# Optimization experiments

Measured on AMD Instinct MI355X. Metric: run time of the kernel, lower is better.

## Reference

```python
import jax, jax.numpy as jnp
import numpy as np

N, E, D_IN, D_H, D_OUT = 100000, 3200000, 256, 256, 64
EPS = 1e-5


def spmm(row, col, w, x, n):
    # y = P @ x where P is sparse with P[row[e], col[e]] = w[e]
    return jax.ops.segment_sum(w[:, None] * x[col], row, num_segments=n)


def bn_eval(x, g, b, m, v):
    return (x - m) * jax.lax.rsqrt(v + EPS) * g + b


def setup_inputs() -> dict:
    key = jax.random.key(0)
    ks = jax.random.split(key, 8)
    return {
        "x": jax.random.normal(ks[0], (N, D_IN), jnp.float32),
        "edge_row": jax.random.randint(ks[1], (E,), 0, N),
        "edge_col": jax.random.randint(ks[2], (E,), 0, N),
        "edge_weight": jax.random.uniform(ks[3], (E,), jnp.float32),
        "W1": jax.random.normal(ks[4], (D_IN, D_H), jnp.float32) * (1.0 / np.sqrt(D_IN)),
        "b1": jnp.zeros((D_H,), jnp.float32),
        "g1": jnp.ones((D_H,), jnp.float32),
        "be1": jnp.zeros((D_H,), jnp.float32),
        "m1": jnp.zeros((D_H,), jnp.float32),
        "v1": jnp.ones((D_H,), jnp.float32),
        "W2": jax.random.normal(ks[5], (D_H, D_H), jnp.float32) * (1.0 / np.sqrt(D_H)),
        "b2": jnp.zeros((D_H,), jnp.float32),
        "g2": jnp.ones((D_H,), jnp.float32),
        "be2": jnp.zeros((D_H,), jnp.float32),
        "m2": jnp.zeros((D_H,), jnp.float32),
        "v2": jnp.ones((D_H,), jnp.float32),
        "W3": jax.random.normal(ks[6], (D_H, D_OUT), jnp.float32) * (1.0 / np.sqrt(D_H)),
        "b3": jnp.zeros((D_OUT,), jnp.float32),
    }


def reference(x, edge_row, edge_col, edge_weight,
              W1, b1, g1, be1, m1, v1,
              W2, b2, g2, be2, m2, v2,
              W3, b3):
    n = x.shape[0]
    # layer 1: linear -> BN(eval) -> SpMM -> relu  (dropout is identity in eval)
    h = x @ W1 + b1
    h = bn_eval(h, g1, be1, m1, v1)
    h = jax.nn.relu(spmm(edge_row, edge_col, edge_weight, h, n))
    # layer 2
    h = h @ W2 + b2
    h = bn_eval(h, g2, be2, m2, v2)
    h = jax.nn.relu(spmm(edge_row, edge_col, edge_weight, h, n))
    # output layer
    h = h @ W3 + b3
    h = spmm(edge_row, edge_col, edge_weight, h, n)
    return jax.nn.log_softmax(h, axis=-1)
```

## Files before the change

kernel.cpp:

```cpp
#include <hip/hip_runtime.h>

#define NN 100000
#define NE 3200000
#define NBUCK 782
#define EPB 8192
#define NCB 391

typedef __attribute__((ext_vector_type(8))) short bf16x8;
typedef __attribute__((ext_vector_type(4))) float f32x4;
typedef __attribute__((ext_vector_type(2))) float f32x2;

__device__ __forceinline__ ushort f2bf(float f) {
  unsigned u = __builtin_bit_cast(unsigned, f);
  u = (u + 0x7FFFu + ((u >> 16) & 1u)) >> 16;
  return (ushort)u;
}
__device__ __forceinline__ float bf2f(ushort h) {
  return __builtin_bit_cast(float, ((unsigned)h) << 16);
}
__device__ __forceinline__ unsigned char f2fp8(float f) {
  return (unsigned char)(__builtin_amdgcn_cvt_pk_fp8_f32(f, 0.f, 0u, false) & 0xFFu);
}
__device__ __forceinline__ float pw2w(unsigned pw) {
  return __builtin_bit_cast(float, (pw & 0x7FFFu) << 16);
}
__device__ __forceinline__ void gl2lds16(const void* g, void* s) {
  __builtin_amdgcn_global_load_lds((const __attribute__((address_space(1))) void*)g,
                                   (__attribute__((address_space(3))) void*)s, 16, 0, 0);
}

__global__ __launch_bounds__(256) void k_cnt(const int* __restrict__ row, int* __restrict__ ghist,
                                             int* __restrict__ bcnt) {
  __shared__ int h[NBUCK];
  int blk = blockIdx.x, tid = threadIdx.x;
  for (int i = tid; i < NBUCK; i += 256) h[i] = 0;
  __syncthreads();
  int lo = blk * EPB, hi = lo + EPB; if (hi > NE) hi = NE;
  for (int i = lo + tid * 4; i < hi; i += 1024) {
    int4 r = *(const int4*)(row + i);
    atomicAdd(&h[r.x >> 7], 1);
    atomicAdd(&h[r.y >> 7], 1);
    atomicAdd(&h[r.z >> 7], 1);
    atomicAdd(&h[r.w >> 7], 1);
  }
  __syncthreads();
  for (int i = tid; i < NBUCK; i += 256) {
    ghist[(size_t)i * NCB + blk] = h[i];
    if (h[i]) atomicAdd(&bcnt[i], h[i]);
  }
}

__global__ __launch_bounds__(1024) void k_bscan(const int* __restrict__ bcnt, int* __restrict__ bbase) {
  __shared__ int s[1024];
  int t = threadIdx.x;
  s[t] = (t < NBUCK) ? bcnt[t] : 0;
  __syncthreads();
  for (int o = 1; o < 1024; o <<= 1) {
    int v = (t >= o) ? s[t - o] : 0;
    __syncthreads();
    s[t] += v;
    __syncthreads();
  }
  if (t < NBUCK) bbase[t] = t ? s[t - 1] : 0;
}

__global__ __launch_bounds__(64) void k_scan3(int* __restrict__ ghist, const int* __restrict__ bbase) {
  int b = blockIdx.x, lane = threadIdx.x;
  int carry = bbase[b];
#pragma unroll
  for (int r = 0; r < 7; ++r) {
    int idx = r * 64 + lane;
    int v = (idx < NCB) ? ghist[(size_t)b * NCB + idx] : 0;
    int s = v;
#pragma unroll
    for (int o = 1; o < 64; o <<= 1) { int t = __shfl_up(s, o, 64); if (lane >= o) s += t; }
    if (idx < NCB) ghist[(size_t)b * NCB + idx] = carry + s - v;
    carry += __shfl(s, 63, 64);
  }
}

__global__ __launch_bounds__(256) void k_place(const int* __restrict__ row, const int* __restrict__ col,
                                               const float* __restrict__ w, const int* __restrict__ ghist,
                                               int2* __restrict__ bdata) {
  __shared__ int offs[NBUCK];
  int blk = blockIdx.x, tid = threadIdx.x;
  for (int i = tid; i < NBUCK; i += 256) offs[i] = ghist[(size_t)i * NCB + blk];
  __syncthreads();
  int lo = blk * EPB, hi = lo + EPB; if (hi > NE) hi = NE;
  for (int i = lo + tid * 4; i < hi; i += 1024) {
    int4 r = *(const int4*)(row + i);
    int4 c = *(const int4*)(col + i);
    float4 ww = *(const float4*)(w + i);
    int p;
    p = atomicAdd(&offs[r.x >> 7], 1); bdata[p] = make_int2(((r.x & 127) << 17) | c.x, __float_as_int(ww.x));
    p = atomicAdd(&offs[r.y >> 7], 1); bdata[p] = make_int2(((r.y & 127) << 17) | c.y, __float_as_int(ww.y));
    p = atomicAdd(&offs[r.z >> 7], 1); bdata[p] = make_int2(((r.z & 127) << 17) | c.z, __float_as_int(ww.z));
    p = atomicAdd(&offs[r.w >> 7], 1); bdata[p] = make_int2(((r.w & 127) << 17) | c.w, __float_as_int(ww.w));
  }
}

__global__ __launch_bounds__(256) void k_bsort(const int* __restrict__ bcnt, const int* __restrict__ bbase,
                                               const int2* __restrict__ bdata, unsigned* __restrict__ cw,
                                               int* __restrict__ rp) {
  __shared__ int sc[128], lpos[128];
  int b = blockIdx.x, t = threadIdx.x;
  int n = bcnt[b], base = bbase[b];
  if (t < 128) sc[t] = 0;
  __syncthreads();
  for (int i = t; i < n; i += 256) {
    int r = bdata[(size_t)base + i].x >> 17;
    atomicAdd(&sc[r], 1);
  }
  __syncthreads();
  for (int o = 1; o < 128; o <<= 1) {
    int v = (t < 128 && t >= o) ? sc[t - o] : 0;
    __syncthreads();
    if (t < 128) sc[t] += v;
    __syncthreads();
  }
  if (t < 128) {
    int excl = t ? sc[t - 1] : 0;
    lpos[t] = excl;
    int grow = b * 128 + t;
    if (grow <= NN) rp[grow] = base + excl;
  }
  __syncthreads();
  for (int i = t; i < n; i += 256) {
    int2 e = bdata[(size_t)base + i];
    int r = e.x >> 17;
    int p = atomicAdd(&lpos[r], 1);
    cw[base + p] = ((unsigned)(e.x & 0x1FFFF) << 15) | (f2bf(__int_as_float(e.y)) & 0x7FFFu);
  }
}

__global__ __launch_bounds__(256) void k_prepall(
    const float* __restrict__ W1, const float* __restrict__ b1, const float* __restrict__ g1,
    const float* __restrict__ be1, const float* __restrict__ m1, const float* __restrict__ v1,
    const float* __restrict__ W2, const float* __restrict__ b2, const float* __restrict__ g2,
    const float* __restrict__ be2, const float* __restrict__ m2, const float* __restrict__ v2,
    const float* __restrict__ W3, const float* __restrict__ b3,
    ushort* __restrict__ W1t, ushort* __restrict__ W2t, ushort* __restrict__ W3t,
    float* __restrict__ bp1, float* __restrict__ bp2, float* __restrict__ bp3,
    int* __restrict__ bcnt) {
  int blk = blockIdx.x, k = threadIdx.x;
  if (blk < 4) { int z = blk * 256 + k; if (z < NBUCK) bcnt[z] = 0; }
  if (blk < 256) {
    int j = blk;
    float s = g1[j] * rsqrtf(v1[j] + 1e-5f), t = be1[j] - m1[j] * s;
    if (k == 0) bp1[j] = b1[j] * s + t;
    W1t[(size_t)j * 256 + k] = f2bf(W1[(size_t)k * 256 + j] * s);
  } else if (blk < 512) {
    int j = blk - 256;
    float s = g2[j] * rsqrtf(v2[j] + 1e-5f), t = be2[j] - m2[j] * s;
    if (k == 0) bp2[j] = b2[j] * s + t;
    W2t[(size_t)j * 256 + k] = f2bf(W2[(size_t)k * 256 + j] * s);
  } else {
    int j = blk - 512;
    if (k == 0) bp3[j] = (j < 64) ? b3[j] : 0.f;
    W3t[(size_t)j * 256 + k] = f2bf((j < 64) ? W3[(size_t)k * 64 + j] : 0.f);
  }
}

__global__ __launch_bounds__(256) void k_gemm1(const float* __restrict__ A, const ushort* __restrict__ Bt,
                                               const float* __restrict__ bp, unsigned char* __restrict__ C,
                                               int M) {
  __shared__ ushort sA[128 * 64];
  __shared__ ushort sB[128 * 64];
  const int tid = threadIdx.x;
  const int lane = tid & 63;
  const int wave = tid >> 6;
  const int wm = wave >> 1, wn = wave & 1;
  const int bm = blockIdx.x, bn = blockIdx.y;

  f32x4 acc[4][4];
#pragma unroll
  for (int a = 0; a < 4; ++a)
#pragma unroll
    for (int b = 0; b < 4; ++b) acc[a][b] = (f32x4){0.f, 0.f, 0.f, 0.f};

  const char* Bb = (const char*)Bt;
  char* sAb = (char*)sA;
  char* sBb = (char*)sB;

  for (int kt = 0; kt < 4; ++kt) {
#pragma unroll
    for (int it = 0; it < 4; ++it) {
      int idx = it * 2048 + tid * 8;
      int row = idx >> 6, colx = idx & 63;
      int ra = bm * 128 + row; if (ra >= M) ra = M - 1;
      const float* src = A + (size_t)ra * 256 + kt * 64 + colx;
      float4 u = *(const float4*)src;
      float4 v = *(const float4*)(src + 4);
      ushort4 r0; r0.x = f2bf(u.x); r0.y = f2bf(u.y); r0.z = f2bf(u.z); r0.w = f2bf(u.w);
      ushort4 r1; r1.x = f2bf(v.x); r1.y = f2bf(v.y); r1.z = f2bf(v.z); r1.w = f2bf(v.w);
      *(ushort4*)(sAb + row * 128 + colx * 2) = r0;
      *(ushort4*)(sAb + row * 128 + colx * 2 + 8) = r1;
    }
#pragma unroll
    for (int it = 0; it < 4; ++it) {
      int o = tid * 16 + it * 4096;
      int r = o >> 7, kb = o & 127;
      gl2lds16(Bb + (size_t)(bn * 128 + r) * 512 + kt * 128 + kb, sBb + o);
    }
    __syncthreads();
#pragma unroll
    for (int kk = 0; kk < 2; ++kk) {
      int kByte = kk * 64 + ((lane >> 4) << 4);
      bf16x8 af[4], bfr[4];
#pragma unroll
      for (int mi = 0; mi < 4; ++mi)
        af[mi] = *(const bf16x8*)(sAb + (wm * 64 + mi * 16 + (lane & 15)) * 128 + kByte);
#pragma unroll
      for (int ni = 0; ni < 4; ++ni)
        bfr[ni] = *(const bf16x8*)(sBb + (wn * 64 + ni * 16 + (lane & 15)) * 128 + kByte);
#pragma unroll
      for (int mi = 0; mi < 4; ++mi)
#pragma unroll
        for (int ni = 0; ni < 4; ++ni)
          acc[mi][ni] = __builtin_amdgcn_mfma_f32_16x16x32_bf16(af[mi], bfr[ni], acc[mi][ni], 0, 0, 0);
    }
    __syncthreads();
  }

  const int r0 = bm * 128 + wm * 64 + ((lane >> 4) << 2);
  const int c0 = bn * 128 + wn * 64 + (lane & 15);
#pragma unroll
  for (int ni = 0; ni < 4; ++ni) {
    int col = c0 + ni * 16;
    float bpv = bp[col];
#pragma unroll
    for (int mi = 0; mi < 4; ++mi)
#pragma unroll
      for (int i = 0; i < 4; ++i) {
        int row = r0 + mi * 16 + i;
        if (row < M) C[(size_t)row * 256 + col] = f2fp8(acc[mi][ni][i] + bpv);
      }
  }
}

__global__ __launch_bounds__(256) void k_gemm(const ushort* __restrict__ A, const ushort* __restrict__ Bt,
                                              const float* __restrict__ bp, unsigned char* __restrict__ C,
                                              int M, int ldc, int ncst) {
  __shared__ ushort sA[128 * 64];
  __shared__ ushort sB[128 * 64];
  const int tid = threadIdx.x;
  const int lane = tid & 63;
  const int wave = tid >> 6;
  const int wm = wave >> 1, wn = wave & 1;
  const int bm = blockIdx.x, bn = blockIdx.y;

  f32x4 acc[4][4];
#pragma unroll
  for (int a = 0; a < 4; ++a)
#pragma unroll
    for (int b = 0; b < 4; ++b) acc[a][b] = (f32x4){0.f, 0.f, 0.f, 0.f};

  const char* Ab = (const char*)A;
  const char* Bb = (const char*)Bt;
  char* sAb = (char*)sA;
  char* sBb = (char*)sB;

  for (int kt = 0; kt < 4; ++kt) {
#pragma unroll
    for (int it = 0; it < 4; ++it) {
      int o = tid * 16 + it * 4096;
      int r = o >> 7, kb = o & 127;
      int ra = bm * 128 + r; if (ra >= M) ra = M - 1;
      gl2lds16(Ab + (size_t)ra * 512 + kt * 128 + kb, sAb + o);
      gl2lds16(Bb + (size_t)(bn * 128 + r) * 512 + kt * 128 + kb, sBb + o);
    }
    __syncthreads();
#pragma unroll
    for (int kk = 0; kk < 2; ++kk) {
      int kByte = kk * 64 + ((lane >> 4) << 4);
      bf16x8 af[4], bfr[4];
#pragma unroll
      for (int mi = 0; mi < 4; ++mi)
        af[mi] = *(const bf16x8*)(sAb + (wm * 64 + mi * 16 + (lane & 15)) * 128 + kByte);
#pragma unroll
      for (int ni = 0; ni < 4; ++ni)
        bfr[ni] = *(const bf16x8*)(sBb + (wn * 64 + ni * 16 + (lane & 15)) * 128 + kByte);
#pragma unroll
      for (int mi = 0; mi < 4; ++mi)
#pragma unroll
        for (int ni = 0; ni < 4; ++ni)
          acc[mi][ni] = __builtin_amdgcn_mfma_f32_16x16x32_bf16(af[mi], bfr[ni], acc[mi][ni], 0, 0, 0);
    }
    __syncthreads();
  }

  const int r0 = bm * 128 + wm * 64 + ((lane >> 4) << 2);
  const int c0 = bn * 128 + wn * 64 + (lane & 15);
#pragma unroll
  for (int ni = 0; ni < 4; ++ni) {
    int col = c0 + ni * 16;
    if (col >= ncst) continue;
    float bpv = bp[col];
#pragma unroll
    for (int mi = 0; mi < 4; ++mi)
#pragma unroll
      for (int i = 0; i < 4; ++i) {
        int row = r0 + mi * 16 + i;
        if (row < M) C[(size_t)row * ldc + col] = f2fp8(acc[mi][ni][i] + bpv);
      }
  }
}

__device__ __forceinline__ void gacc16(const unsigned* __restrict__ cw, int i, int rem,
                                       const char* __restrict__ Hb, f32x2& a01, f32x2& a23) {
  unsigned p[16]; unsigned g[16];
#pragma unroll
  for (int u = 0; u < 16; ++u) p[u] = cw[i + (u < rem ? u : 0)];
#pragma unroll
  for (int u = 0; u < 16; ++u) g[u] = *(const unsigned*)(Hb + ((size_t)(p[u] >> 15) << 8));
#pragma unroll
  for (int u = 0; u < 16; ++u) {
    float wf = (u < rem) ? pw2w(p[u]) : 0.f;
    f32x2 wv = {wf, wf};
    a01 += wv * __builtin_amdgcn_cvt_pk_f32_fp8(g[u], false);
    a23 += wv * __builtin_amdgcn_cvt_pk_f32_fp8(g[u], true);
  }
}

__global__ __launch_bounds__(256) void k_spmm256(const int* __restrict__ rp, const unsigned* __restrict__ cw,
                                                 const unsigned char* __restrict__ H, ushort* __restrict__ Y) {
  int node = blockIdx.x * 4 + (threadIdx.x >> 6);
  int lane = threadIdx.x & 63;
  int s = __builtin_amdgcn_readfirstlane(rp[node]);
  int e = __builtin_amdgcn_readfirstlane(rp[node + 1]);
  f32x2 a01 = {0.f, 0.f}, a23 = {0.f, 0.f};
  const char* Hb = (const char*)H + (lane << 2);
  int i = s;
  for (; i + 16 <= e; i += 16) gacc16(cw, i, 16, Hb, a01, a23);
  int rem = e - i;
  if (rem) gacc16(cw, i, rem, Hb, a01, a23);
  ushort4 o;
  o.x = f2bf(fmaxf(a01.x, 0.f)); o.y = f2bf(fmaxf(a01.y, 0.f));
  o.z = f2bf(fmaxf(a23.x, 0.f)); o.w = f2bf(fmaxf(a23.y, 0.f));
  *(ushort4*)(Y + (size_t)node * 256 + (lane << 2)) = o;
}

__device__ __forceinline__ void gacc64(const unsigned* __restrict__ cw, int i, int rem,
                                       const unsigned char* __restrict__ H, int word, int shift, float& a) {
  unsigned p[16]; unsigned g[16];
#pragma unroll
  for (int u = 0; u < 16; ++u) p[u] = cw[i + (u < rem ? u : 0)];
#pragma unroll
  for (int u = 0; u < 16; ++u)
    g[u] = *(const unsigned*)(H + ((size_t)(p[u] >> 15) << 6) + word);
#pragma unroll
  for (int u = 0; u < 16; ++u) {
    float h = __builtin_amdgcn_cvt_f32_fp8(g[u] >> shift, 0);
    a += ((u < rem) ? pw2w(p[u]) : 0.f) * h;
  }
}

__global__ __launch_bounds__(256) void k_spmm64(const int* __restrict__ rp, const unsigned* __restrict__ cw,
                                                const unsigned char* __restrict__ H, float* __restrict__ out) {
  int node = blockIdx.x * 4 + (threadIdx.x >> 6);
  int lane = threadIdx.x & 63;
  int s = __builtin_amdgcn_readfirstlane(rp[node]);
  int e = __builtin_amdgcn_readfirstlane(rp[node + 1]);
  int word = (lane >> 2) << 2;
  int shift = (lane & 3) << 3;
  float a = 0.f;
  int i = s;
  for (; i + 16 <= e; i += 16) gacc64(cw, i, 16, H, word, shift, a);
  int rem = e - i;
  if (rem) gacc64(cw, i, rem, H, word, shift, a);
  float mx = a;
#pragma unroll
  for (int o = 32; o > 0; o >>= 1) mx = fmaxf(mx, __shfl_xor(mx, o, 64));
  float ex = expf(a - mx);
  float sum = ex;
#pragma unroll
  for (int o = 32; o > 0; o >>= 1) sum += __shfl_xor(sum, o, 64);
  out[(size_t)node * 64 + lane] = (a - mx) - logf(sum);
}

extern "C" void kernel_launch(void* const* d_in, const int* in_sizes, int n_in,
                              void* d_out, int out_size, void* d_ws, size_t ws_size,
                              hipStream_t stream) {
  const float* x   = (const float*)d_in[0];
  const int* erow  = (const int*)d_in[1];
  const int* ecol  = (const int*)d_in[2];
  const float* ew  = (const float*)d_in[3];
  const float* W1  = (const float*)d_in[4];
  const float* b1  = (const float*)d_in[5];
  const float* g1  = (const float*)d_in[6];
  const float* be1 = (const float*)d_in[7];
  const float* m1  = (const float*)d_in[8];
  const float* v1  = (const float*)d_in[9];
  const float* W2  = (const float*)d_in[10];
  const float* b2  = (const float*)d_in[11];
  const float* g2  = (const float*)d_in[12];
  const float* be2 = (const float*)d_in[13];
  const float* m2  = (const float*)d_in[14];
  const float* v2  = (const float*)d_in[15];
  const float* W3  = (const float*)d_in[16];
  const float* b3  = (const float*)d_in[17];

  char* ws = (char*)d_ws;
  size_t off = 0;
  auto carve = [&](size_t bytes) -> void* {
    void* p = ws + off;
    off += (bytes + 511) & ~(size_t)511;
    return p;
  };
  int* bcnt    = (int*)carve((size_t)NBUCK * 4);
  int* bbase   = (int*)carve((size_t)NBUCK * 4);
  int* ghist   = (int*)carve((size_t)NBUCK * NCB * 4);
  int* rp      = (int*)carve((size_t)(NBUCK * 128 + 1) * 4);
  unsigned* cw = (unsigned*)carve((size_t)NE * 4);
  ushort* W1t  = (ushort*)carve(256 * 256 * 2);
  ushort* W2t  = (ushort*)carve(256 * 256 * 2);
  ushort* W3t  = (ushort*)carve(128 * 256 * 2);
  float* bp1   = (float*)carve(256 * 4);
  float* bp2   = (float*)carve(256 * 4);
  float* bp3   = (float*)carve(128 * 4);
  ushort* bufH        = (ushort*)carve((size_t)NN * 256 * 2);
  unsigned char* bufZ = (unsigned char*)carve((size_t)NN * 256);
  unsigned char* bufZ3 = (unsigned char*)carve((size_t)NN * 64);
  if (off > ws_size) return;

  int2* bdata = (int2*)bufH;

  k_prepall<<<640, 256, 0, stream>>>(W1, b1, g1, be1, m1, v1, W2, b2, g2, be2, m2, v2,
                                     W3, b3, W1t, W2t, W3t, bp1, bp2, bp3, bcnt);
  k_cnt<<<NCB, 256, 0, stream>>>(erow, ghist, bcnt);
  k_bscan<<<1, 1024, 0, stream>>>(bcnt, bbase);
  k_scan3<<<NBUCK, 64, 0, stream>>>(ghist, bbase);
  k_place<<<NCB, 256, 0, stream>>>(erow, ecol, ew, ghist, bdata);
  k_bsort<<<NBUCK, 256, 0, stream>>>(bcnt, bbase, bdata, cw, rp);

  const int gm = (NN + 127) / 128;
  k_gemm1<<<dim3(gm, 2), 256, 0, stream>>>(x, W1t, bp1, bufZ, NN);
  k_spmm256<<<NN / 4, 256, 0, stream>>>(rp, cw, bufZ, bufH);
  k_gemm<<<dim3(gm, 2), 256, 0, stream>>>(bufH, W2t, bp2, bufZ, NN, 256, 256);
  k_spmm256<<<NN / 4, 256, 0, stream>>>(rp, cw, bufZ, bufH);
  k_gemm<<<dim3(gm, 1), 256, 0, stream>>>(bufH, W3t, bp3, bufZ3, NN, 64, 64);
  k_spmm64<<<NN / 4, 256, 0, stream>>>(rp, cw, bufZ3, (float*)d_out);
}
```

Measured before the change: 519.1 us.

## Merge preprocessing launches and co-schedule edge placement with first GEMM

Merges weight prep with the bucket histogram kernel and folds the bucket-base scan into k_scan3, where each block sums the preceding bucket counts itself. Edge placement now runs as extra blocks of the first GEMM launch, so the bandwidth-bound scatter overlaps the compute-bound GEMM. This cuts the launch count and the idle gaps between small kernels. In exchange, bcnt is zeroed with a memset, and each scan3 block does redundant prefix sums over up to 782 counts.

```diff
diff --git a/kernel.cpp b/kernel.cpp
--- a/kernel.cpp
+++ b/kernel.cpp
@@ -29,14 +29,40 @@
                                    (__attribute__((address_space(3))) void*)s, 16, 0, 0);
 }
 
-__global__ __launch_bounds__(256) void k_cnt(const int* __restrict__ row, int* __restrict__ ghist,
-                                             int* __restrict__ bcnt) {
+__global__ __launch_bounds__(256) void k_pc(
+    const float* __restrict__ W1, const float* __restrict__ b1, const float* __restrict__ g1,
+    const float* __restrict__ be1, const float* __restrict__ m1, const float* __restrict__ v1,
+    const float* __restrict__ W2, const float* __restrict__ b2, const float* __restrict__ g2,
+    const float* __restrict__ be2, const float* __restrict__ m2, const float* __restrict__ v2,
+    const float* __restrict__ W3, const float* __restrict__ b3,
+    ushort* __restrict__ W1t, ushort* __restrict__ W2t, ushort* __restrict__ W3t,
+    float* __restrict__ bp1, float* __restrict__ bp2, float* __restrict__ bp3,
+    const int* __restrict__ row, int* __restrict__ ghist, int* __restrict__ bcnt) {
   __shared__ int h[NBUCK];
-  int blk = blockIdx.x, tid = threadIdx.x;
-  for (int i = tid; i < NBUCK; i += 256) h[i] = 0;
+  int bid = blockIdx.x, k = threadIdx.x;
+  if (bid < 640) {
+    if (bid < 256) {
+      int j = bid;
+      float s = g1[j] * rsqrtf(v1[j] + 1e-5f), t = be1[j] - m1[j] * s;
+      if (k == 0) bp1[j] = b1[j] * s + t;
+      W1t[(size_t)j * 256 + k] = f2bf(W1[(size_t)k * 256 + j] * s);
+    } else if (bid < 512) {
+      int j = bid - 256;
+      float s = g2[j] * rsqrtf(v2[j] + 1e-5f), t = be2[j] - m2[j] * s;
+      if (k == 0) bp2[j] = b2[j] * s + t;
+      W2t[(size_t)j * 256 + k] = f2bf(W2[(size_t)k * 256 + j] * s);
+    } else {
+      int j = bid - 512;
+      if (k == 0) bp3[j] = (j < 64) ? b3[j] : 0.f;
+      W3t[(size_t)j * 256 + k] = f2bf((j < 64) ? W3[(size_t)k * 64 + j] : 0.f);
+    }
+    return;
+  }
+  int blk = bid - 640;
+  for (int i = k; i < NBUCK; i += 256) h[i] = 0;
   __syncthreads();
   int lo = blk * EPB, hi = lo + EPB; if (hi > NE) hi = NE;
-  for (int i = lo + tid * 4; i < hi; i += 1024) {
+  for (int i = lo + k * 4; i < hi; i += 1024) {
     int4 r = *(const int4*)(row + i);
     atomicAdd(&h[r.x >> 7], 1);
     atomicAdd(&h[r.y >> 7], 1);
@@ -44,29 +70,21 @@
     atomicAdd(&h[r.w >> 7], 1);
   }
   __syncthreads();
-  for (int i = tid; i < NBUCK; i += 256) {
+  for (int i = k; i < NBUCK; i += 256) {
     ghist[(size_t)i * NCB + blk] = h[i];
     if (h[i]) atomicAdd(&bcnt[i], h[i]);
   }
 }
 
-__global__ __launch_bounds__(1024) void k_bscan(const int* __restrict__ bcnt, int* __restrict__ bbase) {
-  __shared__ int s[1024];
-  int t = threadIdx.x;
-  s[t] = (t < NBUCK) ? bcnt[t] : 0;
-  __syncthreads();
-  for (int o = 1; o < 1024; o <<= 1) {
-    int v = (t >= o) ? s[t - o] : 0;
-    __syncthreads();
-    s[t] += v;
-    __syncthreads();
-  }
-  if (t < NBUCK) bbase[t] = t ? s[t - 1] : 0;
-}
-
-__global__ __launch_bounds__(64) void k_scan3(int* __restrict__ ghist, const int* __restrict__ bbase) {
+__global__ __launch_bounds__(64) void k_scan3(int* __restrict__ ghist, const int* __restrict__ bcnt,
+                                              int* __restrict__ bbase) {
   int b = blockIdx.x, lane = threadIdx.x;
-  int carry = bbase[b];
+  int acc = 0;
+  for (int i = lane; i < b; i += 64) acc += bcnt[i];
+#pragma unroll
+  for (int o = 32; o > 0; o >>= 1) acc += __shfl_xor(acc, o, 64);
+  int carry = acc;
+  if (lane == 0) bbase[b] = carry;
 #pragma unroll
   for (int r = 0; r < 7; ++r) {
     int idx = r * 64 + lane;
@@ -79,23 +97,99 @@
   }
 }
 
-__global__ __launch_bounds__(256) void k_place(const int* __restrict__ row, const int* __restrict__ col,
-                                               const float* __restrict__ w, const int* __restrict__ ghist,
-                                               int2* __restrict__ bdata) {
-  __shared__ int offs[NBUCK];
-  int blk = blockIdx.x, tid = threadIdx.x;
-  for (int i = tid; i < NBUCK; i += 256) offs[i] = ghist[(size_t)i * NCB + blk];
-  __syncthreads();
-  int lo = blk * EPB, hi = lo + EPB; if (hi > NE) hi = NE;
-  for (int i = lo + tid * 4; i < hi; i += 1024) {
-    int4 r = *(const int4*)(row + i);
-    int4 c = *(const int4*)(col + i);
-    float4 ww = *(const float4*)(w + i);
-    int p;
-    p = atomicAdd(&offs[r.x >> 7], 1); bdata[p] = make_int2(((r.x & 127) << 17) | c.x, __float_as_int(ww.x));
-    p = atomicAdd(&offs[r.y >> 7], 1); bdata[p] = make_int2(((r.y & 127) << 17) | c.y, __float_as_int(ww.y));
-    p = atomicAdd(&offs[r.z >> 7], 1); bdata[p] = make_int2(((r.z & 127) << 17) | c.z, __float_as_int(ww.z));
-    p = atomicAdd(&offs[r.w >> 7], 1); bdata[p] = make_int2(((r.w & 127) << 17) | c.w, __float_as_int(ww.w));
+__global__ __launch_bounds__(256) void k_pg1(const float* __restrict__ A, const ushort* __restrict__ Bt,
+                                             const float* __restrict__ bp, unsigned char* __restrict__ C,
+                                             const int* __restrict__ row, const int* __restrict__ col,
+                                             const float* __restrict__ w, const int* __restrict__ ghist,
+                                             int2* __restrict__ bdata) {
+  __shared__ char smem[32768];
+  int bid = blockIdx.x;
+  const int tid = threadIdx.x;
+  if (bid >= 1564) {
+    int* offs = (int*)smem;
+    int blk = bid - 1564;
+    for (int i = tid; i < NBUCK; i += 256) offs[i] = ghist[(size_t)i * NCB + blk];
+    __syncthreads();
+    int lo = blk * EPB, hi = lo + EPB; if (hi > NE) hi = NE;
+    for (int i = lo + tid * 4; i < hi; i += 1024) {
+      int4 r = *(const int4*)(row + i);
+      int4 c = *(const int4*)(col + i);
+      float4 ww = *(const float4*)(w + i);
+      int p;
+      p = atomicAdd(&offs[r.x >> 7], 1); bdata[p] = make_int2(((r.x & 127) << 17) | c.x, __float_as_int(ww.x));
+      p = atomicAdd(&offs[r.y >> 7], 1); bdata[p] = make_int2(((r.y & 127) << 17) | c.y, __float_as_int(ww.y));
+      p = atomicAdd(&offs[r.z >> 7], 1); bdata[p] = make_int2(((r.z & 127) << 17) | c.z, __float_as_int(ww.z));
+      p = atomicAdd(&offs[r.w >> 7], 1); bdata[p] = make_int2(((r.w & 127) << 17) | c.w, __float_as_int(ww.w));
+    }
+    return;
+  }
+  char* sAb = smem;
+  char* sBb = smem + 16384;
+  const int lane = tid & 63;
+  const int wave = tid >> 6;
+  const int wm = wave >> 1, wn = wave & 1;
+  const int bm = bid >> 1, bn = bid & 1;
+
+  f32x4 acc[4][4];
+#pragma unroll
+  for (int a = 0; a < 4; ++a)
+#pragma unroll
+    for (int b = 0; b < 4; ++b) acc[a][b] = (f32x4){0.f, 0.f, 0.f, 0.f};
+
+  const char* Bb = (const char*)Bt;
+  for (int kt = 0; kt < 4; ++kt) {
+#pragma unroll
+    for (int it = 0; it < 4; ++it) {
+      int idx = it * 2048 + tid * 8;
+      int r = idx >> 6, colx = idx & 63;
+      int ra = bm * 128 + r; if (ra >= NN) ra = NN - 1;
+      const float* src = A + (size_t)ra * 256 + kt * 64 + colx;
+      float4 u = *(const float4*)src;
+      float4 v = *(const float4*)(src + 4);
+      ushort4 r0; r0.x = f2bf(u.x); r0.y = f2bf(u.y); r0.z = f2bf(u.z); r0.w = f2bf(u.w);
+      ushort4 r1; r1.x = f2bf(v.x); r1.y = f2bf(v.y); r1.z = f2bf(v.z); r1.w = f2bf(v.w);
+      *(ushort4*)(sAb + r * 128 + colx * 2) = r0;
+      *(ushort4*)(sAb + r * 128 + colx * 2 + 8) = r1;
+    }
+#pragma unroll
+    for (int it = 0; it < 4; ++it) {
+      int o = tid * 16 + it * 4096;
+      int r = o >> 7, kb = o & 127;
+      gl2lds16(Bb + (size_t)(bn * 128 + r) * 512 + kt * 128 + kb, sBb + o);
+    }
+    __syncthreads();
+#pragma unroll
+    for (int kk = 0; kk < 2; ++kk) {
+      int kByte = kk * 64 + ((lane >> 4) << 4);
+      bf16x8 af[4], bfr[4];
+#pragma unroll
+      for (int mi = 0; mi < 4; ++mi)
+        af[mi] = *(const bf16x8*)(sAb + (wm * 64 + mi * 16 + (lane & 15)) * 128 + kByte);
+#pragma unroll
+      for (int ni = 0; ni < 4; ++ni)
+        bfr[ni] = *(const bf16x8*)(sBb + (wn * 64 + ni * 16 + (lane & 15)) * 128 + kByte);
+#pragma unroll
+      for (int mi = 0; mi < 4; ++mi)
+#pragma unroll
+        for (int ni = 0; ni < 4; ++ni)
+          acc[mi][ni] = __builtin_amdgcn_mfma_f32_16x16x32_bf16(af[mi], bfr[ni], acc[mi][ni], 0, 0, 0);
+    }
+    __syncthreads();
+  }
+
+  const int r0 = bm * 128 + wm * 64 + ((lane >> 4) << 2);
+  const int c0 = bn * 128 + wn * 64 + (lane & 15);
+#pragma unroll
+  for (int ni = 0; ni < 4; ++ni) {
+    int col2 = c0 + ni * 16;
+    float bpv = bp[col2];
+#pragma unroll
+    for (int mi = 0; mi < 4; ++mi)
+#pragma unroll
+      for (int i = 0; i < 4; ++i) {
+        int r = r0 + mi * 16 + i;
+        if (r < NN) C[(size_t)r * 256 + col2] = f2fp8(acc[mi][ni][i] + bpv);
+      }
   }
 }
 
@@ -130,111 +224,6 @@
     int r = e.x >> 17;
     int p = atomicAdd(&lpos[r], 1);
     cw[base + p] = ((unsigned)(e.x & 0x1FFFF) << 15) | (f2bf(__int_as_float(e.y)) & 0x7FFFu);
-  }
-}
-
-__global__ __launch_bounds__(256) void k_prepall(
-    const float* __restrict__ W1, const float* __restrict__ b1, const float* __restrict__ g1,
-    const float* __restrict__ be1, const float* __restrict__ m1, const float* __restrict__ v1,
-    const float* __restrict__ W2, const float* __restrict__ b2, const float* __restrict__ g2,
-    const float* __restrict__ be2, const float* __restrict__ m2, const float* __restrict__ v2,
-    const float* __restrict__ W3, const float* __restrict__ b3,
-    ushort* __restrict__ W1t, ushort* __restrict__ W2t, ushort* __restrict__ W3t,
-    float* __restrict__ bp1, float* __restrict__ bp2, float* __restrict__ bp3,
-    int* __restrict__ bcnt) {
-  int blk = blockIdx.x, k = threadIdx.x;
-  if (blk < 4) { int z = blk * 256 + k; if (z < NBUCK) bcnt[z] = 0; }
-  if (blk < 256) {
-    int j = blk;
-    float s = g1[j] * rsqrtf(v1[j] + 1e-5f), t = be1[j] - m1[j] * s;
-    if (k == 0) bp1[j] = b1[j] * s + t;
-    W1t[(size_t)j * 256 + k] = f2bf(W1[(size_t)k * 256 + j] * s);
-  } else if (blk < 512) {
-    int j = blk - 256;
-    float s = g2[j] * rsqrtf(v2[j] + 1e-5f), t = be2[j] - m2[j] * s;
-    if (k == 0) bp2[j] = b2[j] * s + t;
-    W2t[(size_t)j * 256 + k] = f2bf(W2[(size_t)k * 256 + j] * s);
-  } else {
-    int j = blk - 512;
-    if (k == 0) bp3[j] = (j < 64) ? b3[j] : 0.f;
-    W3t[(size_t)j * 256 + k] = f2bf((j < 64) ? W3[(size_t)k * 64 + j] : 0.f);
-  }
-}
-
-__global__ __launch_bounds__(256) void k_gemm1(const float* __restrict__ A, const ushort* __restrict__ Bt,
-                                               const float* __restrict__ bp, unsigned char* __restrict__ C,
-                                               int M) {
-  __shared__ ushort sA[128 * 64];
-  __shared__ ushort sB[128 * 64];
-  const int tid = threadIdx.x;
-  const int lane = tid & 63;
-  const int wave = tid >> 6;
-  const int wm = wave >> 1, wn = wave & 1;
-  const int bm = blockIdx.x, bn = blockIdx.y;
-
-  f32x4 acc[4][4];
-#pragma unroll
-  for (int a = 0; a < 4; ++a)
-#pragma unroll
-    for (int b = 0; b < 4; ++b) acc[a][b] = (f32x4){0.f, 0.f, 0.f, 0.f};
-
-  const char* Bb = (const char*)Bt;
-  char* sAb = (char*)sA;
-  char* sBb = (char*)sB;
-
-  for (int kt = 0; kt < 4; ++kt) {
-#pragma unroll
-    for (int it = 0; it < 4; ++it) {
-      int idx = it * 2048 + tid * 8;
-      int row = idx >> 6, colx = idx & 63;
-      int ra = bm * 128 + row; if (ra >= M) ra = M - 1;
-      const float* src = A + (size_t)ra * 256 + kt * 64 + colx;
-      float4 u = *(const float4*)src;
-      float4 v = *(const float4*)(src + 4);
-      ushort4 r0; r0.x = f2bf(u.x); r0.y = f2bf(u.y); r0.z = f2bf(u.z); r0.w = f2bf(u.w);
-      ushort4 r1; r1.x = f2bf(v.x); r1.y = f2bf(v.y); r1.z = f2bf(v.z); r1.w = f2bf(v.w);
-      *(ushort4*)(sAb + row * 128 + colx * 2) = r0;
-      *(ushort4*)(sAb + row * 128 + colx * 2 + 8) = r1;
-    }
-#pragma unroll
-    for (int it = 0; it < 4; ++it) {
-      int o = tid * 16 + it * 4096;
-      int r = o >> 7, kb = o & 127;
-      gl2lds16(Bb + (size_t)(bn * 128 + r) * 512 + kt * 128 + kb, sBb + o);
-    }
-    __syncthreads();
-#pragma unroll
-    for (int kk = 0; kk < 2; ++kk) {
-      int kByte = kk * 64 + ((lane >> 4) << 4);
-      bf16x8 af[4], bfr[4];
-#pragma unroll
-      for (int mi = 0; mi < 4; ++mi)
-        af[mi] = *(const bf16x8*)(sAb + (wm * 64 + mi * 16 + (lane & 15)) * 128 + kByte);
-#pragma unroll
-      for (int ni = 0; ni < 4; ++ni)
-        bfr[ni] = *(const bf16x8*)(sBb + (wn * 64 + ni * 16 + (lane & 15)) * 128 + kByte);
-#pragma unroll
-      for (int mi = 0; mi < 4; ++mi)
-#pragma unroll
-        for (int ni = 0; ni < 4; ++ni)
-          acc[mi][ni] = __builtin_amdgcn_mfma_f32_16x16x32_bf16(af[mi], bfr[ni], acc[mi][ni], 0, 0, 0);
-    }
-    __syncthreads();
-  }
-
-  const int r0 = bm * 128 + wm * 64 + ((lane >> 4) << 2);
-  const int c0 = bn * 128 + wn * 64 + (lane & 15);
-#pragma unroll
-  for (int ni = 0; ni < 4; ++ni) {
-    int col = c0 + ni * 16;
-    float bpv = bp[col];
-#pragma unroll
-    for (int mi = 0; mi < 4; ++mi)
-#pragma unroll
-      for (int i = 0; i < 4; ++i) {
-        int row = r0 + mi * 16 + i;
-        if (row < M) C[(size_t)row * 256 + col] = f2fp8(acc[mi][ni][i] + bpv);
-      }
   }
 }
 
@@ -425,16 +414,14 @@
 
   int2* bdata = (int2*)bufH;
 
-  k_prepall<<<640, 256, 0, stream>>>(W1, b1, g1, be1, m1, v1, W2, b2, g2, be2, m2, v2,
-                                     W3, b3, W1t, W2t, W3t, bp1, bp2, bp3, bcnt);
-  k_cnt<<<NCB, 256, 0, stream>>>(erow, ghist, bcnt);
-  k_bscan<<<1, 1024, 0, stream>>>(bcnt, bbase);
-  k_scan3<<<NBUCK, 64, 0, stream>>>(ghist, bbase);
-  k_place<<<NCB, 256, 0, stream>>>(erow, ecol, ew, ghist, bdata);
+  hipMemsetAsync(bcnt, 0, (size_t)NBUCK * 4, stream);
+  k_pc<<<1031, 256, 0, stream>>>(W1, b1, g1, be1, m1, v1, W2, b2, g2, be2, m2, v2, W3, b3,
+                                 W1t, W2t, W3t, bp1, bp2, bp3, erow, ghist, bcnt);
+  k_scan3<<<NBUCK, 64, 0, stream>>>(ghist, bcnt, bbase);
+  k_pg1<<<1955, 256, 0, stream>>>(x, W1t, bp1, bufZ, erow, ecol, ew, ghist, bdata);
   k_bsort<<<NBUCK, 256, 0, stream>>>(bcnt, bbase, bdata, cw, rp);
 
   const int gm = (NN + 127) / 128;
-  k_gemm1<<<dim3(gm, 2), 256, 0, stream>>>(x, W1t, bp1, bufZ, NN);
   k_spmm256<<<NN / 4, 256, 0, stream>>>(rp, cw, bufZ, bufH);
   k_gemm<<<dim3(gm, 2), 256, 0, stream>>>(bufH, W2t, bp2, bufZ, NN, 256, 256);
   k_spmm256<<<NN / 4, 256, 0, stream>>>(rp, cw, bufZ, bufH);
```

Measured after the change: 515.5 us. Within noise of the previous version (-0.7%).
